# Optimization experiments

Hardware: AMD Instinct MI355X
Metric: run time of the kernel (lower is better)

The kernel has to match this reference:

```python
import jax, jax.numpy as jnp
import numpy as np

N, C, H, W = 4, 256, 64, 64
D = 128  # inter_channels = C // 2


def setup_inputs() -> dict:
    key = jax.random.key(0)
    ks = jax.random.split(key, 9)
    s = 0.05  # weight scale
    return {
        "x": jax.random.normal(ks[0], (N, C, H, W), jnp.float32),
        "Wg": jax.random.normal(ks[1], (D, C), jnp.float32) * s,
        "bg": jax.random.normal(ks[2], (D,), jnp.float32) * s,
        "Wt": jax.random.normal(ks[3], (D, C), jnp.float32) * s,
        "bt": jax.random.normal(ks[4], (D,), jnp.float32) * s,
        "Wp": jax.random.normal(ks[5], (D, C), jnp.float32) * s,
        "bp": jax.random.normal(ks[6], (D,), jnp.float32) * s,
        "Wz": jax.random.normal(ks[7], (C, D), jnp.float32) * s,
        "bz": jax.random.normal(ks[8], (C,), jnp.float32) * s,
    }


def reference(x, Wg, bg, Wt, bt, Wp, bp, Wz, bz):
    # NonLocalBlock, mode='embedded', dimension=2, bn_layer=False.
    # 1x1 convs are per-pixel linear maps over channels.
    n, c, h, w = x.shape
    xf = x.reshape(n, c, h * w)                                  # (N,C,S)
    g_x = jnp.einsum('dc,ncs->nds', Wg, xf) + bg[None, :, None]  # (N,D,S)
    th = jnp.einsum('dc,ncs->nds', Wt, xf) + bt[None, :, None]   # (N,D,S)
    ph = jnp.einsum('dc,ncs->nds', Wp, xf) + bp[None, :, None]   # (N,D,S)
    f = jnp.einsum('nds,ndt->nst', th, ph)                       # (N,S,S)
    att = jax.nn.softmax(f, axis=-1)
    y = jnp.einsum('nst,ndt->nds', att, g_x)                     # (N,D,S)
    w_y = jnp.einsum('cd,nds->ncs', Wz, y) + bz[None, :, None]   # (N,C,S)
    return (w_y + xf).reshape(n, c, h, w)
```

## Files before the change

kernel.cpp:

```cpp
#include <hip/hip_runtime.h>
#include <math.h>

#define N_ 4
#define C_ 256
#define D_ 128
#define S_ 4096
#define LOG2E 1.4426950408889634f
#define SPLIT 4
#define TPS 16

typedef __attribute__((ext_vector_type(4))) float f32x4;
typedef __attribute__((ext_vector_type(16))) float f32x16;
typedef __attribute__((ext_vector_type(8))) short short8;
typedef __attribute__((ext_vector_type(8))) unsigned short ushort8;
typedef __attribute__((ext_vector_type(4))) unsigned short ushort4v;

#define MFMA16(a, b, c) __builtin_amdgcn_mfma_f32_16x16x32_bf16((a), (b), (c), 0, 0, 0)
#define MFMA32(a, b, c) __builtin_amdgcn_mfma_f32_32x32x16_bf16((a), (b), (c), 0, 0, 0)

__device__ __forceinline__ unsigned short f2bf(float f) {
  union { float f; unsigned int u; } v; v.f = f;
  unsigned int r = v.u + 0x7fffu + ((v.u >> 16) & 1u);
  return (unsigned short)(r >> 16);
}
__device__ __forceinline__ float bf2f(unsigned short u) {
  union { unsigned int u; float f; } v; v.u = ((unsigned int)u) << 16;
  return v.f;
}
__device__ __forceinline__ unsigned cvtpk(float lo, float hi) {
  unsigned r;
  asm("v_cvt_pk_bf16_f32 %0, %1, %2" : "=v"(r) : "v"(lo), "v"(hi));
  return r;
}
__device__ __forceinline__ float vsum16(const f32x16& v) {
  float a = (v[0] + v[1]) + (v[2] + v[3]);
  float b = (v[4] + v[5]) + (v[6] + v[7]);
  float c = (v[8] + v[9]) + (v[10] + v[11]);
  float d = (v[12] + v[13]) + (v[14] + v[15]);
  return (a + b) + (c + d);
}
__device__ __forceinline__ void gload16(const void* g, void* l) {
  __builtin_amdgcn_global_load_lds((const __attribute__((address_space(1))) unsigned int*)g,
                                   (__attribute__((address_space(3))) unsigned int*)l,
                                   16, 0, 0);
}

__global__ void k_convw(const float* __restrict__ w0, const float* __restrict__ w1,
                        const float* __restrict__ w2, const float* __restrict__ w3,
                        unsigned short* __restrict__ d0, unsigned short* __restrict__ d1,
                        unsigned short* __restrict__ d2, unsigned short* __restrict__ d3) {
  int b = blockIdx.x;
  int w = b >> 4;
  int i = (b & 15) * 256 + threadIdx.x;
  const float* s = (w == 0) ? w0 : (w == 1) ? w1 : (w == 2) ? w2 : w3;
  unsigned short* d = (w == 0) ? d0 : (w == 1) ? d1 : (w == 2) ? d2 : d3;
  const float4* sp = reinterpret_cast<const float4*>(s) + (size_t)i * 2;
  float4 a = sp[0], c = sp[1];
  ushort8 o;
  o[0] = f2bf(a.x); o[1] = f2bf(a.y); o[2] = f2bf(a.z); o[3] = f2bf(a.w);
  o[4] = f2bf(c.x); o[5] = f2bf(c.y); o[6] = f2bf(c.z); o[7] = f2bf(c.w);
  reinterpret_cast<ushort8*>(d)[i] = o;
}

__global__ __launch_bounds__(256, 3) void k_proj(
    const float* __restrict__ x,
    const unsigned short* __restrict__ wg, const unsigned short* __restrict__ wt,
    const unsigned short* __restrict__ wp,
    const float* __restrict__ bg, const float* __restrict__ bt, const float* __restrict__ bp,
    unsigned short* __restrict__ qb, unsigned short* __restrict__ kb, unsigned short* __restrict__ vb)
{
  __shared__ __align__(16) unsigned short xs[C_ * 64];
  const int tid = threadIdx.x;
  const int p = blockIdx.x >> 8;
  const int n = (blockIdx.x >> 6) & 3;
  const int s0 = (blockIdx.x & 63) << 6;
  const float* xsrc = x + (size_t)n * C_ * S_ + s0;
#pragma unroll
  for (int i = 0; i < 16; ++i) {
    int ch = i * 256 + tid;
    int c = ch >> 4, s4 = (ch & 15) << 2;
    float4 v = *reinterpret_cast<const float4*>(xsrc + (size_t)c * S_ + s4);
    ushort4v o;
    o[0] = f2bf(v.x); o[1] = f2bf(v.y); o[2] = f2bf(v.z); o[3] = f2bf(v.w);
    *reinterpret_cast<ushort4v*>(xs + c * 64 + s4) = o;
  }
  __syncthreads();
  const int lane = tid & 63, wid = tid >> 6;
  const int l15 = lane & 15, g = lane >> 4;
  const int scol = wid * 16 + l15;

  short8 bx[8];
#pragma unroll
  for (int kc = 0; kc < 8; ++kc) {
    int cb = kc * 32 + g * 8;
    short8 t;
#pragma unroll
    for (int j = 0; j < 8; ++j) t[j] = (short)xs[(cb + j) * 64 + scol];
    bx[kc] = t;
  }

  const unsigned short* W = (p == 0) ? wg : ((p == 1) ? wt : wp);
  const float* bias = (p == 0) ? bg : ((p == 1) ? bt : bp);
  const float osc = (p == 1) ? LOG2E : 1.0f;
  const f32x4 fz = {0.f, 0.f, 0.f, 0.f};
  f32x4 acc[8];
#pragma unroll
  for (int dt = 0; dt < 8; ++dt) acc[dt] = fz;
#pragma unroll
  for (int dt = 0; dt < 8; ++dt) {
    const unsigned short* wrow = W + (size_t)(dt * 16 + l15) * C_ + g * 8;
#pragma unroll
    for (int kc = 0; kc < 8; ++kc) {
      short8 a = *reinterpret_cast<const short8*>(wrow + kc * 32);
      acc[dt] = MFMA16(a, bx[kc], acc[dt]);
    }
  }
  if (p == 0) {
#pragma unroll
    for (int dt = 0; dt < 8; ++dt) {
#pragma unroll
      for (int r = 0; r < 4; ++r) {
        int d = dt * 16 + 4 * g + r;
        vb[((size_t)n * D_ + d) * S_ + s0 + scol] = f2bf(acc[dt][r] + bias[d]);
      }
    }
  } else {
    unsigned short* dst = (p == 1) ? qb : kb;
    unsigned short* row = dst + ((size_t)(n * S_) + s0 + scol) * D_;
#pragma unroll
    for (int dt = 0; dt < 8; ++dt) {
      ushort4v o;
#pragma unroll
      for (int r = 0; r < 4; ++r)
        o[r] = f2bf((acc[dt][r] + bias[dt * 16 + 4 * g + r]) * osc);
      *reinterpret_cast<ushort4v*>(row + dt * 16 + 4 * g) = o;
    }
  }
}

__global__ __launch_bounds__(256, 2) void k_attn(
    const unsigned short* __restrict__ qb, const unsigned short* __restrict__ kb,
    const unsigned short* __restrict__ vb,
    unsigned short* __restrict__ opart, float2* __restrict__ ml)
{
  __shared__ __align__(16) unsigned short ksm[2][64 * 128];
  __shared__ __align__(16) unsigned short vsm[2][128 * 64];
  const int tid = threadIdx.x, lane = tid & 63, w = tid >> 6;
  const int l31 = lane & 31, hi = lane >> 5;
  const int b = blockIdx.x;
  const int sp = b & 3, qt = (b >> 2) & 31, n = b >> 7;
  const int q0 = qt << 7;

  unsigned koff[4], voff[4], ubo[4];
#pragma unroll
  for (int j = 0; j < 4; ++j) {
    int f = j * 256 + tid;
    int kr = f >> 4, kc = f & 15;
    koff[j] = kr * D_ + ((kc ^ (kr & 7)) << 3);
    int vr = f >> 3, vc = f & 7;
    voff[j] = vr * S_ + ((vc ^ (vr & 7)) << 3);
    ubo[j] = (unsigned)(j * 256 + (tid & 192)) * 8;
  }
  const unsigned short* kb0 = kb + ((size_t)n * S_ + (size_t)sp * TPS * 64) * D_;
  const unsigned short* vb0 = vb + (size_t)n * D_ * S_ + sp * TPS * 64;

  auto stage = [&](int buf, int t) {
    const unsigned short* kt = kb0 + (size_t)t * 64 * D_;
    const unsigned short* vt = vb0 + t * 64;
#pragma unroll
    for (int j = 0; j < 4; ++j) gload16(kt + koff[j], &ksm[buf][ubo[j]]);
#pragma unroll
    for (int j = 0; j < 4; ++j) gload16(vt + voff[j], &vsm[buf][ubo[j]]);
  };

  stage(0, 0);

  const unsigned short* qsrc = qb + ((size_t)(n * S_) + q0 + w * 32 + l31) * D_;
  short8 qf[8];
#pragma unroll
  for (int k = 0; k < 8; ++k)
    qf[k] = *reinterpret_cast<const short8*>(qsrc + k * 16 + hi * 8);

  const f32x16 z16 = {0.f,0.f,0.f,0.f,0.f,0.f,0.f,0.f,0.f,0.f,0.f,0.f,0.f,0.f,0.f,0.f};
  f32x16 oacc[4];
#pragma unroll
  for (int db = 0; db < 4; ++db) oacc[db] = z16;
  float l_ = 0.f;

  __syncthreads();
  int cur = 0;
  f32x16 pA, pB;

  {
    const unsigned short* ksb = ksm[0];
    pA = z16; pB = z16;
    __builtin_amdgcn_s_setprio(1);
#pragma unroll
    for (int ks = 0; ks < 8; ++ks) {
      int c = ks * 2 + hi;
      int r0 = l31, r1 = 32 + l31;
      short8 k0 = *reinterpret_cast<const short8*>(ksb + r0 * 128 + ((c ^ (r0 & 7)) << 3));
      short8 k1 = *reinterpret_cast<const short8*>(ksb + r1 * 128 + ((c ^ (r1 & 7)) << 3));
      pA = MFMA32(k0, qf[ks], pA);
      pB = MFMA32(k1, qf[ks], pB);
    }
    __builtin_amdgcn_s_setprio(0);
  }

  for (int t = 0; t < TPS; ++t) {
    if (t + 1 < TPS) stage(cur ^ 1, t + 1);

#pragma unroll
    for (int i = 0; i < 16; ++i) pA[i] = exp2f(pA[i]);
#pragma unroll
    for (int i = 0; i < 16; ++i) pB[i] = exp2f(pB[i]);
    l_ += vsum16(pA) + vsum16(pB);

    short8 pa[4];
#pragma unroll
    for (int ks = 0; ks < 4; ++ks) {
      const f32x16& p = (ks < 2) ? pA : pB;
      int ba = (ks & 1) * 8;
      unsigned u0 = cvtpk(p[ba + 0], p[ba + 1]);
      unsigned u1 = cvtpk(p[ba + 2], p[ba + 3]);
      unsigned u2 = cvtpk(p[ba + 4], p[ba + 5]);
      unsigned u3 = cvtpk(p[ba + 6], p[ba + 7]);
      asm("v_permlane32_swap_b32 %0, %1" : "+v"(u0), "+v"(u2));
      asm("v_permlane32_swap_b32 %0, %1" : "+v"(u1), "+v"(u3));
      union { unsigned u[4]; short8 s; } mm;
      mm.u[0] = u0; mm.u[1] = u1; mm.u[2] = u2; mm.u[3] = u3;
      pa[ks] = mm.s;
    }

    {
      const unsigned short* vsb = vsm[cur];
      __builtin_amdgcn_s_setprio(1);
#pragma unroll
      for (int ks = 0; ks < 4; ++ks) {
        int c = ks * 2 + hi;
#pragma unroll
        for (int db = 0; db < 4; ++db) {
          int r = db * 32 + l31;
          short8 v = *reinterpret_cast<const short8*>(vsb + r * 64 + ((c ^ (r & 7)) << 3));
          oacc[db] = MFMA32(pa[ks], v, oacc[db]);
        }
      }
      __builtin_amdgcn_s_setprio(0);
    }

    __syncthreads();

    if (t + 1 < TPS) {
      cur ^= 1;
      const unsigned short* ksb = ksm[cur];
      pA = z16; pB = z16;
      __builtin_amdgcn_s_setprio(1);
#pragma unroll
      for (int ks = 0; ks < 8; ++ks) {
        int c = ks * 2 + hi;
        int r0 = l31, r1 = 32 + l31;
        short8 k0 = *reinterpret_cast<const short8*>(ksb + r0 * 128 + ((c ^ (r0 & 7)) << 3));
        short8 k1 = *reinterpret_cast<const short8*>(ksb + r1 * 128 + ((c ^ (r1 & 7)) << 3));
        pA = MFMA32(k0, qf[ks], pA);
        pB = MFMA32(k1, qf[ks], pB);
      }
      __builtin_amdgcn_s_setprio(0);
    }
  }

  float lrow = l_ + __shfl_xor(l_, 32);
  float linv = 1.f / lrow;
  unsigned short* ob = opart + (((size_t)(n * SPLIT + sp)) * S_ + q0 + w * 32) * D_;
#pragma unroll
  for (int reg = 0; reg < 16; ++reg) {
    int rr = (reg & 3) + 8 * (reg >> 2) + 4 * hi;
    float li = __shfl(linv, rr);
#pragma unroll
    for (int db = 0; db < 4; ++db)
      ob[(size_t)rr * D_ + db * 32 + l31] = f2bf(oacc[db][reg] * li);
  }
  if (hi == 0) {
    ml[((size_t)(n * SPLIT + sp)) * S_ + q0 + w * 32 + l31] = make_float2(0.f, lrow);
  }
}

__global__ __launch_bounds__(256, 2) void k_final(
    const unsigned short* __restrict__ opart, const float2* __restrict__ ml,
    const unsigned short* __restrict__ wz, const float* __restrict__ bz,
    const float* __restrict__ x, float* __restrict__ out)
{
  __shared__ __align__(16) unsigned short ysm[32 * 128];
  __shared__ float wsm[32][4];
  const int tid = threadIdx.x, lane = tid & 63, wid = tid >> 6;
  const int l15 = lane & 15, g = lane >> 4;
  const int n = blockIdx.x >> 7, s0 = (blockIdx.x & 127) << 5;

  if (tid < 32) {
    int row = s0 + tid;
    float mv[4], lv[4];
    float M = -3.4e38f;
#pragma unroll
    for (int i = 0; i < 4; ++i) {
      float2 v = ml[(size_t)(n * 4 + i) * S_ + row];
      mv[i] = v.x; lv[i] = v.y;
      M = fmaxf(M, mv[i]);
    }
    float wsum = 0.f, wv[4];
#pragma unroll
    for (int i = 0; i < 4; ++i) { wv[i] = lv[i] * exp2f((mv[i] - M) * LOG2E); wsum += wv[i]; }
    float L = 1.f / wsum;
#pragma unroll
    for (int i = 0; i < 4; ++i) wsm[tid][i] = wv[i] * L;
  }
  __syncthreads();

#pragma unroll
  for (int i = 0; i < 2; ++i) {
    int ch = i * 256 + tid;
    int row = ch >> 4, d8 = ch & 15;
    const unsigned short* p = opart + ((size_t)(n * 4) * S_ + s0 + row) * D_ + d8 * 8;
    float acc[8] = {0.f, 0.f, 0.f, 0.f, 0.f, 0.f, 0.f, 0.f};
#pragma unroll
    for (int j = 0; j < 4; ++j) {
      ushort8 a = *reinterpret_cast<const ushort8*>(p + (size_t)j * S_ * D_);
      float wj = wsm[row][j];
#pragma unroll
      for (int e = 0; e < 8; ++e) acc[e] += bf2f(a[e]) * wj;
    }
    ushort8 o;
#pragma unroll
    for (int e = 0; e < 8; ++e) o[e] = f2bf(acc[e]);
    *reinterpret_cast<ushort8*>(ysm + row * 128 + ((d8 ^ (row & 7)) << 3)) = o;
  }
  __syncthreads();

  const int c0 = wid * 64;
  const f32x4 fz = {0.f, 0.f, 0.f, 0.f};
  f32x4 acc[4][2];
#pragma unroll
  for (int ct = 0; ct < 4; ++ct)
#pragma unroll
    for (int st = 0; st < 2; ++st) acc[ct][st] = fz;
#pragma unroll
  for (int kc = 0; kc < 4; ++kc) {
    short8 by[2];
#pragma unroll
    for (int st = 0; st < 2; ++st) {
      int r = st * 16 + l15;
      int ch = (kc * 4 + g) ^ (r & 7);
      by[st] = *reinterpret_cast<const short8*>(ysm + r * 128 + ch * 8);
    }
#pragma unroll
    for (int ct = 0; ct < 4; ++ct) {
      const short8 aw = *reinterpret_cast<const short8*>(
          wz + (size_t)(c0 + ct * 16 + l15) * D_ + kc * 32 + g * 8);
#pragma unroll
      for (int st = 0; st < 2; ++st) acc[ct][st] = MFMA16(aw, by[st], acc[ct][st]);
    }
  }
#pragma unroll
  for (int ct = 0; ct < 4; ++ct)
#pragma unroll
    for (int r = 0; r < 4; ++r) {
      int c = c0 + ct * 16 + 4 * g + r;
      float bias = bz[c];
#pragma unroll
      for (int st = 0; st < 2; ++st) {
        int s = s0 + st * 16 + l15;
        size_t idx = ((size_t)(n * C_ + c)) * S_ + s;
        out[idx] = acc[ct][st][r] + bias + x[idx];
      }
    }
}

extern "C" void kernel_launch(void* const* d_in, const int* in_sizes, int n_in,
                              void* d_out, int out_size, void* d_ws, size_t ws_size,
                              hipStream_t stream) {
  const float* x  = (const float*)d_in[0];
  const float* Wg = (const float*)d_in[1];
  const float* bg = (const float*)d_in[2];
  const float* Wt = (const float*)d_in[3];
  const float* bt = (const float*)d_in[4];
  const float* Wp = (const float*)d_in[5];
  const float* bp = (const float*)d_in[6];
  const float* Wz = (const float*)d_in[7];
  const float* bz = (const float*)d_in[8];
  float* out = (float*)d_out;
  char* ws = (char*)d_ws;
  const size_t MB = 1u << 20;
  unsigned short* qb    = (unsigned short*)(ws);
  unsigned short* kb    = (unsigned short*)(ws + 4 * MB);
  unsigned short* vb    = (unsigned short*)(ws + 8 * MB);
  unsigned short* opart = (unsigned short*)(ws + 12 * MB);
  float2*        mlbuf  = (float2*)(ws + 28 * MB);
  unsigned short* wgb   = (unsigned short*)(ws + 28 * MB + 524288);
  unsigned short* wtb   = (unsigned short*)(ws + 28 * MB + 524288 + 65536);
  unsigned short* wpb   = (unsigned short*)(ws + 28 * MB + 524288 + 131072);
  unsigned short* wzb   = (unsigned short*)(ws + 28 * MB + 524288 + 196608);

  k_convw<<<64, 256, 0, stream>>>(Wg, Wt, Wp, Wz, wgb, wtb, wpb, wzb);
  k_proj <<<768, 256, 0, stream>>>(x, wgb, wtb, wpb, bg, bt, bp, qb, kb, vb);
  k_attn <<<512, 256, 0, stream>>>(qb, kb, vb, opart, mlbuf);
  k_final<<<512, 256, 0, stream>>>(opart, mlbuf, wzb, bz, x, out);
}
```

Measured before the change: 92.68 us.

## Store K in MFMA fragment layout and load it directly from global

The projection kernel now writes K into a pre-swizzled per-fragment layout matching the 32x32x16 MFMA operand order. The attention kernel then reads K fragments straight from global memory with coalesced 16-byte loads, dropping the K shared-memory staging buffer and its LDS traffic. This halves LDS usage per block and may raise occupancy. The cost is that K loads now sit on the critical path before the QK MFMAs with no prefetch, so global/L2 latency is exposed on every tile.

Result: slower. 110.7 us (+19.4%).

```diff
diff --git a/kernel.cpp b/kernel.cpp
--- a/kernel.cpp
+++ b/kernel.cpp
@@ -67,7 +67,8 @@
     const unsigned short* __restrict__ wg, const unsigned short* __restrict__ wt,
     const unsigned short* __restrict__ wp,
     const float* __restrict__ bg, const float* __restrict__ bt, const float* __restrict__ bp,
-    unsigned short* __restrict__ qb, unsigned short* __restrict__ kb, unsigned short* __restrict__ vb)
+    unsigned short* __restrict__ qb, unsigned short* __restrict__ kfrag,
+    unsigned short* __restrict__ vb)
 {
   __shared__ __align__(16) unsigned short xs[C_ * 64];
   const int tid = threadIdx.x;
@@ -124,9 +125,8 @@
         vb[((size_t)n * D_ + d) * S_ + s0 + scol] = f2bf(acc[dt][r] + bias[d]);
       }
     }
-  } else {
-    unsigned short* dst = (p == 1) ? qb : kb;
-    unsigned short* row = dst + ((size_t)(n * S_) + s0 + scol) * D_;
+  } else if (p == 1) {
+    unsigned short* row = qb + ((size_t)(n * S_) + s0 + scol) * D_;
 #pragma unroll
     for (int dt = 0; dt < 8; ++dt) {
       ushort4v o;
@@ -135,15 +135,27 @@
         o[r] = f2bf((acc[dt][r] + bias[dt * 16 + 4 * g + r]) * osc);
       *reinterpret_cast<ushort4v*>(row + dt * 16 + 4 * g) = o;
     }
+  } else {
+    int row_s = s0 + scol;
+    int kvblk = row_s >> 5, lrow = row_s & 31;
+#pragma unroll
+    for (int dt = 0; dt < 8; ++dt) {
+      ushort4v o;
+#pragma unroll
+      for (int r = 0; r < 4; ++r)
+        o[r] = f2bf(acc[dt][r] + bias[dt * 16 + 4 * g + r]);
+      size_t off = ((((size_t)n * 128 + kvblk) * 8 + dt) * 64 + (g >> 1) * 32 + lrow) * 8
+                   + (g & 1) * 4;
+      *reinterpret_cast<ushort4v*>(kfrag + off) = o;
+    }
   }
 }
 
 __global__ __launch_bounds__(256, 2) void k_attn(
-    const unsigned short* __restrict__ qb, const unsigned short* __restrict__ kb,
+    const unsigned short* __restrict__ qb, const unsigned short* __restrict__ kfrag,
     const unsigned short* __restrict__ vb,
     unsigned short* __restrict__ opart, float2* __restrict__ ml)
 {
-  __shared__ __align__(16) unsigned short ksm[2][64 * 128];
   __shared__ __align__(16) unsigned short vsm[2][128 * 64];
   const int tid = threadIdx.x, lane = tid & 63, w = tid >> 6;
   const int l31 = lane & 31, hi = lane >> 5;
@@ -151,24 +163,19 @@
   const int sp = b & 3, qt = (b >> 2) & 31, n = b >> 7;
   const int q0 = qt << 7;
 
-  unsigned koff[4], voff[4], ubo[4];
+  unsigned voff[4], ubo[4];
 #pragma unroll
   for (int j = 0; j < 4; ++j) {
     int f = j * 256 + tid;
-    int kr = f >> 4, kc = f & 15;
-    koff[j] = kr * D_ + ((kc ^ (kr & 7)) << 3);
     int vr = f >> 3, vc = f & 7;
     voff[j] = vr * S_ + ((vc ^ (vr & 7)) << 3);
     ubo[j] = (unsigned)(j * 256 + (tid & 192)) * 8;
   }
-  const unsigned short* kb0 = kb + ((size_t)n * S_ + (size_t)sp * TPS * 64) * D_;
   const unsigned short* vb0 = vb + (size_t)n * D_ * S_ + sp * TPS * 64;
+  const unsigned short* kf0 = kfrag + (((size_t)n * 128 + sp * 32) * 8) * 512 + lane * 8;
 
   auto stage = [&](int buf, int t) {
-    const unsigned short* kt = kb0 + (size_t)t * 64 * D_;
     const unsigned short* vt = vb0 + t * 64;
-#pragma unroll
-    for (int j = 0; j < 4; ++j) gload16(kt + koff[j], &ksm[buf][ubo[j]]);
 #pragma unroll
     for (int j = 0; j < 4; ++j) gload16(vt + voff[j], &vsm[buf][ubo[j]]);
   };
@@ -192,15 +199,13 @@
   f32x16 pA, pB;
 
   {
-    const unsigned short* ksb = ksm[0];
+    const unsigned short* kt = kf0;
     pA = z16; pB = z16;
     __builtin_amdgcn_s_setprio(1);
 #pragma unroll
     for (int ks = 0; ks < 8; ++ks) {
-      int c = ks * 2 + hi;
-      int r0 = l31, r1 = 32 + l31;
-      short8 k0 = *reinterpret_cast<const short8*>(ksb + r0 * 128 + ((c ^ (r0 & 7)) << 3));
-      short8 k1 = *reinterpret_cast<const short8*>(ksb + r1 * 128 + ((c ^ (r1 & 7)) << 3));
+      short8 k0 = *reinterpret_cast<const short8*>(kt + ks * 512);
+      short8 k1 = *reinterpret_cast<const short8*>(kt + (8 + ks) * 512);
       pA = MFMA32(k0, qf[ks], pA);
       pB = MFMA32(k1, qf[ks], pB);
     }
@@ -252,15 +257,13 @@
 
     if (t + 1 < TPS) {
       cur ^= 1;
-      const unsigned short* ksb = ksm[cur];
+      const unsigned short* kt = kf0 + (size_t)(2 * (t + 1)) * 8 * 512;
       pA = z16; pB = z16;
       __builtin_amdgcn_s_setprio(1);
 #pragma unroll
       for (int ks = 0; ks < 8; ++ks) {
-        int c = ks * 2 + hi;
-        int r0 = l31, r1 = 32 + l31;
-        short8 k0 = *reinterpret_cast<const short8*>(ksb + r0 * 128 + ((c ^ (r0 & 7)) << 3));
-        short8 k1 = *reinterpret_cast<const short8*>(ksb + r1 * 128 + ((c ^ (r1 & 7)) << 3));
+        short8 k0 = *reinterpret_cast<const short8*>(kt + ks * 512);
+        short8 k1 = *reinterpret_cast<const short8*>(kt + (8 + ks) * 512);
         pA = MFMA32(k0, qf[ks], pA);
         pB = MFMA32(k1, qf[ks], pB);
       }
```
